# Kernel optimization log

Hardware: AMD Instinct MI355X
Metric: run time of the kernel (lower is better)

## Reference

```python
import jax, jax.numpy as jnp
import numpy as np

B, K = 262144, 101
ALPHA = 0.5
W_ESE, W_EMD, W_TAIL, W_LPEAK, W_UNI = 2.0, 2.0, 5.0, 5.0, 1.5
LOCAL_MARGIN = 0.25


def setup_inputs() -> dict:
    key = jax.random.key(0)
    k1, k2 = jax.random.split(key)
    logit = jax.random.normal(k1, (B, K), dtype=jnp.float32)
    true_labels = jax.random.randint(k2, (B,), 0, K, dtype=jnp.int32)
    class_weights = jnp.ones((K,), dtype=jnp.float32)
    return {"logit": logit, "true_labels": true_labels, "class_weights": class_weights}


def _ordinal_loss(logit, class_weights, true_labels):
    Bn, Kn = logit.shape
    inv_logK = 1.0 / np.log(float(Kn))
    inv_Km1 = 1.0 / (Kn - 1)
    j = jnp.arange(Kn)

    # CE (class-weighted, reduction='none' then mean), normalized by log K
    logp = jax.nn.log_softmax(logit, axis=1)
    w_y = class_weights[true_labels]                      # [B]
    logp_y = jnp.take_along_axis(logp, true_labels[:, None], axis=1)[:, 0]
    ce_loss = jnp.mean(-w_y * logp_y) * inv_logK

    probs = jnp.exp(logp)                                 # softmax probs [B, K]

    # ESE: expected squared normalized distance, class-weighted
    dist = jnp.abs(j[None, :] - true_labels[:, None]).astype(probs.dtype) * inv_Km1  # [B, K]
    ese = jnp.mean((probs * dist * dist).sum(axis=1) * w_y)

    # EMD: squared CDF mismatch (cdf_true row y = tril ones -> 1 where j <= y)
    cdf_pred = jnp.cumsum(probs, axis=1)
    cdf_true = (j[None, :] <= true_labels[:, None]).astype(probs.dtype)
    emd = jnp.mean(((cdf_pred - cdf_true) ** 2).sum(axis=1) / Kn)

    # Tail: mass at |j - y| > 1
    tail_mask = (jnp.abs(j[None, :] - true_labels[:, None]) > 1).astype(probs.dtype)
    tail = jnp.mean((probs * tail_mask).sum(axis=1))

    # Local peak: relu(max(p[y-1], p[y+1]) - (p[y] - margin))
    py = jnp.take_along_axis(probs, true_labels[:, None], axis=1)[:, 0]
    li = jnp.maximum(true_labels - 1, 0)[:, None]
    ri = jnp.minimum(true_labels + 1, Kn - 1)[:, None]
    py_left = jnp.where(true_labels > 0,
                        jnp.take_along_axis(probs, li, axis=1)[:, 0], 0.0)
    py_right = jnp.where(true_labels + 1 < Kn,
                         jnp.take_along_axis(probs, ri, axis=1)[:, 0], 0.0)
    local_peak = jnp.mean(jax.nn.relu(jnp.maximum(py_left, py_right) - (py - LOCAL_MARGIN)))

    # Unimodal: vectorized form of the per-distance loop.
    # Left of y: relu(p[m] - p[m+1]) for m < y ; right of y: relu(p[m+1] - p[m]) for m >= y.
    # Total violation count is exactly B*(K-1) (y left terms + K-1-y right terms per sample).
    m = jnp.arange(Kn - 1)
    left_mask = (m[None, :] < true_labels[:, None]).astype(probs.dtype)
    right_mask = 1.0 - left_mask
    dl = jax.nn.relu(probs[:, :-1] - probs[:, 1:])
    dr = jax.nn.relu(probs[:, 1:] - probs[:, :-1])
    total_viols = (dl * left_mask).sum() + (dr * right_mask).sum()
    unimodal = total_viols / (Bn * (Kn - 1))

    ord_block = (W_ESE * ese + W_EMD * emd + W_TAIL * tail
                 + W_LPEAK * local_peak + W_UNI * unimodal)
    return ce_loss + ALPHA * ord_block


def reference(logit, true_labels, class_weights):
    return _ordinal_loss(logit, class_weights, true_labels)
```

## Files before the change

### kernel.cpp

```cpp
#include <hip/hip_runtime.h>
#include <math.h>
#include <stdint.h>

#define BROWS 262144
#define KCLS  101
#define ROWB  404
#define RPB   16
#define BATCHB (RPB * ROWB)
#define STAGEB 7168
#define NBPW  8
#define NWAVE (BROWS / (RPB * NBPW))
#define TOTB  (BROWS * ROWB)

typedef const __attribute__((address_space(1))) uint32_t* gptr_t;
typedef __attribute__((address_space(3))) uint32_t*       lptr_t;

__device__ __forceinline__ void stage_batch(const char* base, unsigned off,
                                            char* dst, int lane) {
#pragma unroll
    for (int k = 0; k < 7; ++k) {
        unsigned o = off + (unsigned)(k * 1024 + lane * 16);
        o = (o > (unsigned)(TOTB - 16)) ? (unsigned)(TOTB - 16) : o;
        __builtin_amdgcn_global_load_lds((gptr_t)(base + o),
                                         (lptr_t)(dst + k * 1024), 16, 0, 0);
    }
}

extern "C" __global__ void __launch_bounds__(64)
ord_main(const float* __restrict__ logit,
         const int*   __restrict__ labels,
         const float* __restrict__ cw,
         float*       __restrict__ partial)
{
    __shared__ __align__(16) char  smem[2 * STAGEB];
    __shared__ __align__(16) int   ylds[128];
    __shared__ __align__(16) float cwlds[128];

    const int lane = threadIdx.x;
    const int q    = lane & 3;
    const int g    = lane >> 2;
    const char* gb = (const char*)logit;
    const unsigned woff = (unsigned)blockIdx.x * (unsigned)(RPB * NBPW * ROWB);

    stage_batch(gb, woff, smem, lane);
    {
        const char* lb = (const char*)labels + (size_t)blockIdx.x * (RPB * NBPW * 4);
        __builtin_amdgcn_global_load_lds((gptr_t)(lb + lane * 4), (lptr_t)ylds, 4, 0, 0);
        __builtin_amdgcn_global_load_lds((gptr_t)(lb + 256 + lane * 4),
                                         (lptr_t)((char*)ylds + 256), 4, 0, 0);
        const char* cwb = (const char*)cw;
        unsigned o1 = 256u + (unsigned)(lane * 4); o1 = (o1 > 400u) ? 400u : o1;
        __builtin_amdgcn_global_load_lds((gptr_t)(cwb + lane * 4), (lptr_t)cwlds, 4, 0, 0);
        __builtin_amdgcn_global_load_lds((gptr_t)(cwb + o1),
                                         (lptr_t)((char*)cwlds + 256), 4, 0, 0);
    }

    const float inv_logK = 1.0f / logf(101.0f);
    const float invK     = 1.0f / 101.0f;
    const int   t0 = 25 * q;
    const int   nn = (q == 3) ? 26 : 25;
    const float nq = (float)nn;

    float tacc = 0.0f;

    for (int k = 0; k < NBPW; ++k) {
        if (k + 1 < NBPW) {
            stage_batch(gb, woff + (unsigned)((k + 1) * BATCHB),
                        smem + ((k + 1) & 1) * STAGEB, lane);
            asm volatile("s_waitcnt vmcnt(7)" ::: "memory");
        } else {
            asm volatile("s_waitcnt vmcnt(0)" ::: "memory");
        }

        const float* rowb = (const float*)(smem + (k & 1) * STAGEB) + g * KCLS;
        const float* lrow = rowb + t0;
        const int    y    = ylds[k * 16 + g];
        const float  wy   = cwlds[y];
        const float  yf   = (float)y;

        float a = 0.f, w = 0.f, sp = 0.f, tl = 0.f, bm = 0.f, cm = 0.f;
        float us = 0.f, ef = 0.f, ep = 0.f;
#pragma unroll
        for (int i = 0; i < 25; ++i) {
            const int   t = t0 + i;
            const float e = __expf(lrow[i]);
            if (i == 0) ef = e; else us += __builtin_fabsf(e - ep);
            a += e;
            w += a;
            sp = __builtin_fmaf(a, a, sp);
            tl += (t <= y) ? a : 0.0f;
            bm = __builtin_fmaf(e, (float)t, bm);
            cm = __builtin_fmaf(e, (float)(t * t), cm);
            ep = e;
        }
        if (q == 3) {
            const float e = __expf(lrow[25]);
            us += __builtin_fabsf(e - ep);
            a += e; w += a;
            sp = __builtin_fmaf(a, a, sp);
            tl += (y >= 100) ? a : 0.0f;
            bm = __builtin_fmaf(e, 100.0f, bm);
            cm = __builtin_fmaf(e, 10000.0f, cm);
            ep = e;
        }

        float incl = a;
        { float u = __shfl_up(incl, 1, 4); incl += (q >= 1) ? u : 0.0f; }
        { float u = __shfl_up(incl, 2, 4); incl += (q >= 2) ? u : 0.0f; }
        const float S   = __shfl(incl, 3, 4);
        const float E   = incl - a;
        const float inv = __builtin_amdgcn_rcpf(S);
        const float nf  = __shfl_down(ef, 1, 4);

        int mi = y - t0 + 1; mi = (mi < 0) ? 0 : mi; mi = (mi > nn) ? nn : mi;
        const float spc  = __builtin_fmaf(nq * E, E, __builtin_fmaf(2.0f * E, w, sp));
        const float tlc  = __builtin_fmaf((float)mi, E, tl);
        const float eseC = __builtin_fmaf(yf, __builtin_fmaf(yf, a, -2.0f * bm), cm);
        const float uniC = us + ((q < 3) ? __builtin_fabsf(ep - nf) : 0.0f)
                         + ((q == 0) ? ef : 0.0f) + ((q == 3) ? ep : 0.0f);

        float part = (wy * 1.0e-4f * inv) * eseC;
        part = __builtin_fmaf(invK * inv * inv, spc, part);
        part = __builtin_fmaf(-2.0f * invK * inv, tlc, part);
        part = __builtin_fmaf(0.00375f * inv, uniC, part);
        part += __shfl_xor(part, 1);
        part += __shfl_xor(part, 2);

        const int   ym = (y > 0)   ? y - 1 : 0;
        const int   yp = (y < 100) ? y + 1 : 100;
        const float xy = rowb[y];
        const float eY = __expf(xy);
        const float eL = (y > 0)   ? __expf(rowb[ym]) : 0.0f;
        const float eR = (y < 100) ? __expf(rowb[yp]) : 0.0f;
        const float lnS  = __logf(S);
        const float py   = eY * inv;
        const float tail = 1.0f - (eL + eY + eR) * inv;
        const float lp   = fmaxf(__builtin_fmaf(fmaxf(eL, eR), inv, 0.25f - py), 0.0f);
        const float extra = wy * (lnS - xy) * inv_logK
                          + 2.5f * (tail + lp)
                          - 0.0075f * py
                          + invK * (float)(y + 1);

        tacc += (q == 0) ? (part + extra) : 0.0f;
    }

    tacc += __shfl_xor(tacc, 1);
    tacc += __shfl_xor(tacc, 2);
    tacc += __shfl_xor(tacc, 4);
    tacc += __shfl_xor(tacc, 8);
    tacc += __shfl_xor(tacc, 16);
    tacc += __shfl_xor(tacc, 32);

    if (lane == 0) partial[blockIdx.x] = tacc;
}

extern "C" __global__ void __launch_bounds__(256)
ord_final(const float* __restrict__ partial, float* __restrict__ out, int n)
{
    float v = 0.0f;
    for (int i = threadIdx.x; i < n; i += 256) v += partial[i];

    v += __shfl_xor(v, 1);
    v += __shfl_xor(v, 2);
    v += __shfl_xor(v, 4);
    v += __shfl_xor(v, 8);
    v += __shfl_xor(v, 16);
    v += __shfl_xor(v, 32);

    __shared__ float sb[4];
    const int lane = threadIdx.x & 63;
    const int wid  = threadIdx.x >> 6;
    if (lane == 0) sb[wid] = v;
    __syncthreads();
    if (threadIdx.x == 0)
        out[0] = ((sb[0] + sb[1]) + (sb[2] + sb[3])) * (1.0f / (float)BROWS);
}

extern "C" void kernel_launch(void* const* d_in, const int* in_sizes, int n_in,
                              void* d_out, int out_size, void* d_ws, size_t ws_size,
                              hipStream_t stream)
{
    const float* logit  = (const float*)d_in[0];
    const int*   labels = (const int*)d_in[1];
    const float* cw     = (const float*)d_in[2];
    float*       part   = (float*)d_ws;

    hipLaunchKernelGGL(ord_main, dim3(NWAVE), dim3(64), 0, stream,
                       logit, labels, cw, part);
    hipLaunchKernelGGL(ord_final, dim3(1), dim3(256), 0, stream,
                       part, (float*)d_out, NWAVE);
}
```

Before: 29.11 us.

## Switch to persistent grid-stride blocks with double-buffered label staging

Replaces the fixed 2048 one-wave blocks, each covering 8 contiguous 16-row batches, with 2560 persistent blocks that stride across all 16384 batches. Labels are now staged per batch into a double buffer alongside the logits, and the wait count is adjusted for the extra load. The goal is better load balance and occupancy across the CUs and a longer pipeline per block. In exchange each block's accesses become strided rather than contiguous, and the workspace-size clamp (NB) is computed but never used.

```diff
diff --git a/kernel.cpp b/kernel.cpp
--- a/kernel.cpp
+++ b/kernel.cpp
@@ -8,9 +8,10 @@
 #define RPB   16
 #define BATCHB (RPB * ROWB)
 #define STAGEB 7168
-#define NBPW  8
-#define NWAVE (BROWS / (RPB * NBPW))
 #define TOTB  (BROWS * ROWB)
+#define NBT   (BROWS / RPB)
+#define NBLK  2560
+#define LBLB  (BROWS * 4)
 
 typedef const __attribute__((address_space(1))) uint32_t* gptr_t;
 typedef __attribute__((address_space(3))) uint32_t*       lptr_t;
@@ -33,21 +34,26 @@
          float*       __restrict__ partial)
 {
     __shared__ __align__(16) char  smem[2 * STAGEB];
-    __shared__ __align__(16) int   ylds[128];
+    __shared__ __align__(16) int   ylds[2][64];
     __shared__ __align__(16) float cwlds[128];
 
     const int lane = threadIdx.x;
     const int q    = lane & 3;
     const int g    = lane >> 2;
     const char* gb = (const char*)logit;
-    const unsigned woff = (unsigned)blockIdx.x * (unsigned)(RPB * NBPW * ROWB);
-
-    stage_batch(gb, woff, smem, lane);
+    const char* lb = (const char*)labels;
+
+    auto stage_labels = [&](int bt, int buf) {
+        unsigned o = (unsigned)bt * 64u + (unsigned)(lane * 4);
+        o = (o > (unsigned)(LBLB - 4)) ? (unsigned)(LBLB - 4) : o;
+        __builtin_amdgcn_global_load_lds((gptr_t)(lb + o), (lptr_t)&ylds[buf][0], 4, 0, 0);
+    };
+
+    const int bt0 = blockIdx.x;
+
+    stage_batch(gb, (unsigned)bt0 * (unsigned)BATCHB, smem, lane);
+    stage_labels(bt0, 0);
     {
-        const char* lb = (const char*)labels + (size_t)blockIdx.x * (RPB * NBPW * 4);
-        __builtin_amdgcn_global_load_lds((gptr_t)(lb + lane * 4), (lptr_t)ylds, 4, 0, 0);
-        __builtin_amdgcn_global_load_lds((gptr_t)(lb + 256 + lane * 4),
-                                         (lptr_t)((char*)ylds + 256), 4, 0, 0);
         const char* cwb = (const char*)cw;
         unsigned o1 = 256u + (unsigned)(lane * 4); o1 = (o1 > 400u) ? 400u : o1;
         __builtin_amdgcn_global_load_lds((gptr_t)(cwb + lane * 4), (lptr_t)cwlds, 4, 0, 0);
@@ -62,19 +68,22 @@
     const float nq = (float)nn;
 
     float tacc = 0.0f;
-
-    for (int k = 0; k < NBPW; ++k) {
-        if (k + 1 < NBPW) {
-            stage_batch(gb, woff + (unsigned)((k + 1) * BATCHB),
-                        smem + ((k + 1) & 1) * STAGEB, lane);
-            asm volatile("s_waitcnt vmcnt(7)" ::: "memory");
+    int cur = 0;
+
+    for (int bt = bt0; bt < NBT; bt += NBLK) {
+        const int nxt = bt + NBLK;
+        if (nxt < NBT) {
+            stage_batch(gb, (unsigned)nxt * (unsigned)BATCHB,
+                        smem + (cur ^ 1) * STAGEB, lane);
+            stage_labels(nxt, cur ^ 1);
+            asm volatile("s_waitcnt vmcnt(8)" ::: "memory");
         } else {
             asm volatile("s_waitcnt vmcnt(0)" ::: "memory");
         }
 
-        const float* rowb = (const float*)(smem + (k & 1) * STAGEB) + g * KCLS;
+        const float* rowb = (const float*)(smem + cur * STAGEB) + g * KCLS;
         const float* lrow = rowb + t0;
-        const int    y    = ylds[k * 16 + g];
+        const int    y    = ylds[cur][g];
         const float  wy   = cwlds[y];
         const float  yf   = (float)y;
 
@@ -142,6 +151,7 @@
                           + invK * (float)(y + 1);
 
         tacc += (q == 0) ? (part + extra) : 0.0f;
+        cur ^= 1;
     }
 
     tacc += __shfl_xor(tacc, 1);
@@ -185,8 +195,13 @@
     const float* cw     = (const float*)d_in[2];
     float*       part   = (float*)d_ws;
 
-    hipLaunchKernelGGL(ord_main, dim3(NWAVE), dim3(64), 0, stream,
+    int NB = NBLK;
+    if ((size_t)NB * sizeof(float) > ws_size) NB = (int)(ws_size / sizeof(float));
+    if (NB > NBLK) NB = NBLK;
+    if (NB < 1) NB = 1;
+
+    hipLaunchKernelGGL(ord_main, dim3(NBLK), dim3(64), 0, stream,
                        logit, labels, cw, part);
     hipLaunchKernelGGL(ord_final, dim3(1), dim3(256), 0, stream,
-                       part, (float*)d_out, NWAVE);
-}
+                       part, (float*)d_out, NBLK);
+}
```

After: 32.22 us. +10.7%, slower.
